# Kernel tuning notes

Hardware: AMD Instinct MI355X
Metric: run time of the kernel (lower is better)

The kernel has to match this reference:

```python
import jax, jax.numpy as jnp
import numpy as np

ALPHA = 0.25
GAMMA = 2
IGNORE_INDEX = 255
LOSS_WEIGHT = 1.0
NUM_CLASSES = 19


def setup_inputs() -> dict:
    key = jax.random.key(0)
    k1, k2 = jax.random.split(key)
    N, C, H, W = 4, NUM_CLASSES, 512, 512
    cls_score = jax.random.normal(k1, (N, C, H, W), dtype=jnp.float32)
    label = jax.random.randint(k2, (N, H, W), 0, NUM_CLASSES, dtype=jnp.int64)
    return {"cls_score": cls_score, "label": label}


def reference(cls_score, label):
    # _expand_onehot_labels: valid pixels get a one-hot channel vector
    valid = (label >= 0) & (label != IGNORE_INDEX)          # [N,H,W]
    safe_lab = jnp.where(valid, label, 0)
    onehot = jax.nn.one_hot(safe_lab, cls_score.shape[1], axis=1,
                            dtype=cls_score.dtype)          # [N,C,H,W]
    validf = valid.astype(cls_score.dtype)[:, None, :, :]   # [N,1,H,W]
    onehot = onehot * validf

    # Focal class weight. NOTE: the original torch code uses the RAW logits
    # (temp_pred = pred.cpu()), not sigmoid(pred), when computing the weight.
    x = cls_score
    class_weight = jnp.where(onehot == 1,
                             ALPHA * (1.0 - x) ** GAMMA,
                             ALPHA * x ** GAMMA)            # [N,C,H,W]

    # binary_cross_entropy_with_logits, reduction='none', weight=class_weight
    bce = jnp.maximum(x, 0) - x * onehot + jnp.log1p(jnp.exp(-jnp.abs(x)))
    loss = bce * class_weight

    # weight_reduce_loss with weight=valid_mask (expanded), reduction='mean'
    loss = (loss * validf).mean()
    return LOSS_WEIGHT * loss
```

## Files before the change

### kernel.cpp

```cpp
#include <hip/hip_runtime.h>


#define NC 19
#define IGNORE_INDEX 255
#define ALPHA 0.25f

constexpr int NBATCH = 4;
constexpr int HW = 512 * 512;
constexpr int QPP = HW / 4;
constexpr int NQUADS = NBATCH * QPP;
constexpr int BLOCK = 256;
constexpr int GRID = NQUADS / BLOCK;
constexpr float INV_TOTAL = 1.0f / (float)(NBATCH * NC * HW);

__device__ __forceinline__ float block_reduce(float v, float* smem) {
    #pragma unroll
    for (int off = 32; off > 0; off >>= 1)
        v += __shfl_down(v, off, 64);
    const int lane = threadIdx.x & 63;
    const int wid  = threadIdx.x >> 6;
    if (lane == 0) smem[wid] = v;
    __syncthreads();
    float s = 0.0f;
    if (threadIdx.x == 0) {
        const int nw = blockDim.x >> 6;
        for (int i = 0; i < nw; ++i) s += smem[i];
    }
    return s;
}

__global__ __launch_bounds__(BLOCK) void focal_partial(
        const float* __restrict__ x,
        const int*   __restrict__ label,
        float*       __restrict__ partial) {
    const int q = blockIdx.x * blockDim.x + threadIdx.x;
    const int n  = q / QPP;
    const int pq = q - n * QPP;

    const int4 l4 = *reinterpret_cast<const int4*>(label + (size_t)n * HW + (size_t)pq * 4);
    int   lab[4]   = {l4.x, l4.y, l4.z, l4.w};
    bool  valid[4];
    #pragma unroll
    for (int j = 0; j < 4; ++j)
        valid[j] = (lab[j] >= 0) && (lab[j] != IGNORE_INDEX);

    const float* base = x + (size_t)n * NC * HW + (size_t)pq * 4;

    float acc = 0.0f;
    for (int c = 0; c < NC; ++c) {
        const float4 v = *reinterpret_cast<const float4*>(base + (size_t)c * HW);
        float xs[4] = {v.x, v.y, v.z, v.w};
        #pragma unroll
        for (int j = 0; j < 4; ++j) {
            if (valid[j]) {
                const float xv = xs[j];
                const bool  t  = (lab[j] == c);
                const float d  = t ? (1.0f - xv) : xv;
                const float w  = ALPHA * d * d;
                const float sp  = __logf(1.0f + __expf(-fabsf(xv)));
                const float bce = fmaxf(xv, 0.0f) - (t ? xv : 0.0f) + sp;
                acc += bce * w;
            }
        }
    }

    __shared__ float smem[BLOCK / 64];
    const float s = block_reduce(acc, smem);
    if (threadIdx.x == 0) partial[blockIdx.x] = s;
}

__global__ __launch_bounds__(BLOCK) void focal_finalize(
        const float* __restrict__ partial,
        float*       __restrict__ out) {
    float acc = 0.0f;
    for (int i = threadIdx.x; i < GRID; i += BLOCK)
        acc += partial[i];
    __shared__ float smem[BLOCK / 64];
    const float s = block_reduce(acc, smem);
    if (threadIdx.x == 0) out[0] = s * INV_TOTAL;
}

extern "C" void kernel_launch(void* const* d_in, const int* in_sizes, int n_in,
                              void* d_out, int out_size, void* d_ws, size_t ws_size,
                              hipStream_t stream) {
    const float* cls_score = (const float*)d_in[0];
    const int*   label     = (const int*)d_in[1];
    float* out     = (float*)d_out;
    float* partial = (float*)d_ws;

    focal_partial<<<GRID, BLOCK, 0, stream>>>(cls_score, label, partial);
    focal_finalize<<<1, BLOCK, 0, stream>>>(partial, out);
}
```

Measured before the change: 25.75 us.

## Fuse finalize into main kernel via last-block atomic counter, prefetch all channels

Replaces the separate finalize kernel with a last-block-done pattern: each block writes its partial, bumps an atomic counter, and the last block reduces all partials. All 19 channel float4 loads are issued up front into registers, and the per-pixel valid branch becomes a select. A memset of the counter is added per launch, and the larger register footprint may reduce occupancy.

```diff
diff --git a/kernel.cpp b/kernel.cpp
--- a/kernel.cpp
+++ b/kernel.cpp
@@ -19,65 +19,77 @@
         v += __shfl_down(v, off, 64);
     const int lane = threadIdx.x & 63;
     const int wid  = threadIdx.x >> 6;
+    __syncthreads();
     if (lane == 0) smem[wid] = v;
     __syncthreads();
     float s = 0.0f;
     if (threadIdx.x == 0) {
-        const int nw = blockDim.x >> 6;
-        for (int i = 0; i < nw; ++i) s += smem[i];
+        #pragma unroll
+        for (int i = 0; i < BLOCK / 64; ++i) s += smem[i];
     }
     return s;
 }
 
-__global__ __launch_bounds__(BLOCK) void focal_partial(
+__global__ __launch_bounds__(BLOCK) void focal_fused(
         const float* __restrict__ x,
         const int*   __restrict__ label,
-        float*       __restrict__ partial) {
-    const int q = blockIdx.x * blockDim.x + threadIdx.x;
-    const int n  = q / QPP;
-    const int pq = q - n * QPP;
+        float*       __restrict__ partial,
+        unsigned int* __restrict__ counter,
+        float*       __restrict__ out) {
+    const int q  = blockIdx.x * blockDim.x + threadIdx.x;
+    const int n  = q >> 16;
+    const int pq = q & (QPP - 1);
 
     const int4 l4 = *reinterpret_cast<const int4*>(label + (size_t)n * HW + (size_t)pq * 4);
-    int   lab[4]   = {l4.x, l4.y, l4.z, l4.w};
-    bool  valid[4];
+    const int lab[4] = {l4.x, l4.y, l4.z, l4.w};
+    bool valid[4];
     #pragma unroll
     for (int j = 0; j < 4; ++j)
         valid[j] = (lab[j] >= 0) && (lab[j] != IGNORE_INDEX);
 
     const float* base = x + (size_t)n * NC * HW + (size_t)pq * 4;
 
+    float4 v[NC];
+    #pragma unroll
+    for (int c = 0; c < NC; ++c)
+        v[c] = *reinterpret_cast<const float4*>(base + (size_t)c * HW);
+
     float acc = 0.0f;
+    #pragma unroll
     for (int c = 0; c < NC; ++c) {
-        const float4 v = *reinterpret_cast<const float4*>(base + (size_t)c * HW);
-        float xs[4] = {v.x, v.y, v.z, v.w};
+        const float xs[4] = {v[c].x, v[c].y, v[c].z, v[c].w};
         #pragma unroll
         for (int j = 0; j < 4; ++j) {
-            if (valid[j]) {
-                const float xv = xs[j];
-                const bool  t  = (lab[j] == c);
-                const float d  = t ? (1.0f - xv) : xv;
-                const float w  = ALPHA * d * d;
-                const float sp  = __logf(1.0f + __expf(-fabsf(xv)));
-                const float bce = fmaxf(xv, 0.0f) - (t ? xv : 0.0f) + sp;
-                acc += bce * w;
-            }
+            const float xv = xs[j];
+            const bool  t  = (lab[j] == c);
+            const float d  = t ? (1.0f - xv) : xv;
+            const float w  = ALPHA * d * d;
+            const float sp  = __logf(1.0f + __expf(-fabsf(xv)));
+            const float bce = fmaxf(xv, 0.0f) - (t ? xv : 0.0f) + sp;
+            acc += valid[j] ? bce * w : 0.0f;
         }
     }
 
     __shared__ float smem[BLOCK / 64];
     const float s = block_reduce(acc, smem);
-    if (threadIdx.x == 0) partial[blockIdx.x] = s;
-}
 
-__global__ __launch_bounds__(BLOCK) void focal_finalize(
-        const float* __restrict__ partial,
-        float*       __restrict__ out) {
-    float acc = 0.0f;
-    for (int i = threadIdx.x; i < GRID; i += BLOCK)
-        acc += partial[i];
-    __shared__ float smem[BLOCK / 64];
-    const float s = block_reduce(acc, smem);
-    if (threadIdx.x == 0) out[0] = s * INV_TOTAL;
+    __shared__ bool is_last;
+    if (threadIdx.x == 0) {
+        partial[blockIdx.x] = s;
+        __threadfence();
+        const unsigned int old = atomicAdd(counter, 1u);
+        is_last = (old == GRID - 1);
+    }
+    __syncthreads();
+
+    if (is_last) {
+        __threadfence();
+        float a2 = 0.0f;
+        for (int i = threadIdx.x; i < GRID; i += BLOCK)
+            a2 += partial[i];
+        const float s2 = block_reduce(a2, smem);
+        if (threadIdx.x == 0) out[0] = s2 * INV_TOTAL;
+    }
 }
 
 extern "C" void kernel_launch(void* const* d_in, const int* in_sizes, int n_in,
@@ -85,9 +97,10 @@
                               hipStream_t stream) {
     const float* cls_score = (const float*)d_in[0];
     const int*   label     = (const int*)d_in[1];
-    float* out     = (float*)d_out;
-    float* partial = (float*)d_ws;
+    float* out      = (float*)d_out;
+    float* partial  = (float*)d_ws;
+    unsigned int* counter = (unsigned int*)((char*)d_ws + GRID * sizeof(float));
 
-    focal_partial<<<GRID, BLOCK, 0, stream>>>(cls_score, label, partial);
-    focal_finalize<<<1, BLOCK, 0, stream>>>(partial, out);
+    hipMemsetAsync(counter, 0, sizeof(unsigned int), stream);
+    focal_fused<<<GRID, BLOCK, 0, stream>>>(cls_score, label, partial, counter, out);
 }
```

After: 54.04 us. 2.1x slower.

## Parallelize focal loss over class planes instead of looping classes per thread

Applied to the files above, without the earlier changes.

Each block now processes one (batch, class) plane slice, with every thread loading one float4 of logits plus the matching labels, instead of each thread looping over all 19 classes. This raises the number of blocks and independent memory requests to improve latency hiding. In exchange, labels are re-read once per class and the finalize kernel must sum many more partials, which it does with a 1024-thread block.

```diff
diff --git a/kernel.cpp b/kernel.cpp
--- a/kernel.cpp
+++ b/kernel.cpp
@@ -7,12 +7,13 @@
 
 constexpr int NBATCH = 4;
 constexpr int HW = 512 * 512;
-constexpr int QPP = HW / 4;
-constexpr int NQUADS = NBATCH * QPP;
 constexpr int BLOCK = 256;
-constexpr int GRID = NQUADS / BLOCK;
+constexpr int BPP = HW / (BLOCK * 4);
+constexpr int GRID = NBATCH * NC * BPP;
+constexpr int BLOCK2 = 1024;
 constexpr float INV_TOTAL = 1.0f / (float)(NBATCH * NC * HW);
 
+template <int NWAVE>
 __device__ __forceinline__ float block_reduce(float v, float* smem) {
     #pragma unroll
     for (int off = 32; off > 0; off >>= 1)
@@ -23,8 +24,8 @@
     __syncthreads();
     float s = 0.0f;
     if (threadIdx.x == 0) {
-        const int nw = blockDim.x >> 6;
-        for (int i = 0; i < nw; ++i) s += smem[i];
+        #pragma unroll
+        for (int i = 0; i < NWAVE; ++i) s += smem[i];
     }
     return s;
 }
@@ -33,50 +34,47 @@
         const float* __restrict__ x,
         const int*   __restrict__ label,
         float*       __restrict__ partial) {
-    const int q = blockIdx.x * blockDim.x + threadIdx.x;
-    const int n  = q / QPP;
-    const int pq = q - n * QPP;
+    const int b     = blockIdx.x;
+    const int plane = b >> 8;
+    const int k     = b & 255;
+    const int c     = plane % NC;
+    const int n     = plane / NC;
+    const int pix   = (k << 10) + (threadIdx.x << 2);
 
-    const int4 l4 = *reinterpret_cast<const int4*>(label + (size_t)n * HW + (size_t)pq * 4);
-    int   lab[4]   = {l4.x, l4.y, l4.z, l4.w};
-    bool  valid[4];
-    #pragma unroll
-    for (int j = 0; j < 4; ++j)
-        valid[j] = (lab[j] >= 0) && (lab[j] != IGNORE_INDEX);
-
-    const float* base = x + (size_t)n * NC * HW + (size_t)pq * 4;
+    const float4 v  = *reinterpret_cast<const float4*>(
+                          x + ((size_t)plane << 18) + pix);
+    const int4   l4 = *reinterpret_cast<const int4*>(
+                          label + ((size_t)n << 18) + pix);
+    const int lab[4] = {l4.x, l4.y, l4.z, l4.w};
+    const float xs[4] = {v.x, v.y, v.z, v.w};
 
     float acc = 0.0f;
-    for (int c = 0; c < NC; ++c) {
-        const float4 v = *reinterpret_cast<const float4*>(base + (size_t)c * HW);
-        float xs[4] = {v.x, v.y, v.z, v.w};
-        #pragma unroll
-        for (int j = 0; j < 4; ++j) {
-            if (valid[j]) {
-                const float xv = xs[j];
-                const bool  t  = (lab[j] == c);
-                const float d  = t ? (1.0f - xv) : xv;
-                const float w  = ALPHA * d * d;
-                const float sp  = __logf(1.0f + __expf(-fabsf(xv)));
-                const float bce = fmaxf(xv, 0.0f) - (t ? xv : 0.0f) + sp;
-                acc += bce * w;
-            }
-        }
+    #pragma unroll
+    for (int j = 0; j < 4; ++j) {
+        const float xv   = xs[j];
+        const bool  val  = (lab[j] >= 0) && (lab[j] != IGNORE_INDEX);
+        const bool  t    = (lab[j] == c);
+        const float d    = t ? (1.0f - xv) : xv;
+        float w          = ALPHA * d * d;
+        w                = val ? w : 0.0f;
+        const float sp   = __logf(1.0f + __expf(-fabsf(xv)));
+        const float bce  = fmaxf(xv, 0.0f) - (t ? xv : 0.0f) + sp;
+        acc = fmaf(bce, w, acc);
     }
 
     __shared__ float smem[BLOCK / 64];
-    const float s = block_reduce(acc, smem);
-    if (threadIdx.x == 0) partial[blockIdx.x] = s;
+    const float s = block_reduce<BLOCK / 64>(acc, smem);
+    if (threadIdx.x == 0) partial[b] = s;
 }
 
-__global__ __launch_bounds__(BLOCK) void focal_finalize(
+__global__ __launch_bounds__(BLOCK2) void focal_finalize(
         const float* __restrict__ partial,
         float*       __restrict__ out) {
     float acc = 0.0f;
-    for (int i = threadIdx.x; i < GRID; i += BLOCK)
+    for (int i = threadIdx.x; i < GRID; i += BLOCK2)
         acc += partial[i];
-    __shared__ float smem[BLOCK / 64];
-    const float s = block_reduce(acc, smem);
+    __shared__ float smem[BLOCK2 / 64];
+    const float s = block_reduce<BLOCK2 / 64>(acc, smem);
     if (threadIdx.x == 0) out[0] = s * INV_TOTAL;
 }
 
@@ -89,5 +87,5 @@
     float* partial = (float*)d_ws;
 
     focal_partial<<<GRID, BLOCK, 0, stream>>>(cls_score, label, partial);
-    focal_finalize<<<1, BLOCK, 0, stream>>>(partial, out);
+    focal_finalize<<<1, BLOCK2, 0, stream>>>(partial, out);
 }
```

Measured after the change: 28.39 us. +10.3%, slower.
